# Kernel tuning notes

Measured on AMD Instinct MI355X. Metric: run time of the kernel, lower is better.

Reference implementation:

```python
import jax, jax.numpy as jnp
import numpy as np

T, B, D, H = 512, 64, 1024, 1024


def setup_inputs() -> dict:
    key = jax.random.key(0)
    ks = jax.random.split(key, 7)
    stdv = 1.0 / np.sqrt(H)
    u = lambda k, shape: jax.random.uniform(k, shape, jnp.float32, -stdv, stdv)
    return {
        "x": jax.random.normal(ks[0], (T, B, D), jnp.float32),
        "h0": jax.random.normal(ks[1], (B, H), jnp.float32),
        "c0": jax.random.normal(ks[2], (B, H), jnp.float32),
        "w_ih": u(ks[3], (4 * H, D)),
        "b_ih": u(ks[4], (4 * H,)),
        "w_hh": u(ks[5], (4 * H, H)),
        "b_hh": u(ks[6], (4 * H,)),
    }


def reference(x, h0, c0, w_ih, b_ih, w_hh, b_hh):
    # Precompute input projection for all timesteps in one big GEMM: [T,B,4H]
    gates_x = jnp.einsum("tbd,gd->tbg", x, w_ih) + b_ih

    def step(carry, gx_t):
        h, c = carry
        gates = gx_t + h @ w_hh.T + b_hh  # [B, 4H]
        i_in, f_in, g_in, o_in = jnp.split(gates, 4, axis=1)
        i_t = jax.nn.sigmoid(i_in)
        f_t = jax.nn.sigmoid(f_in)
        g_t = jnp.tanh(g_in)
        o_t = jax.nn.sigmoid(o_in)
        c_t = f_t * c + i_t * g_t
        h_t = o_t * jnp.tanh(c_t)
        return (h_t, c_t), h_t

    (h_n, c_n), hs = jax.lax.scan(step, (h0, c0), gates_x)
    # output: [T, B, H]; final states: [B, H]
    return hs, h_n, c_n
```

## Files before the change

### kernel.cpp

```cpp
#include <hip/hip_runtime.h>

#define TT 512
#define NB 64
#define DD 1024
#define NG 4096

typedef __attribute__((ext_vector_type(8))) __bf16 bf16x8;
typedef __attribute__((ext_vector_type(4))) float f32x4;

#define WC_OFF   0ul
#define HBUF_OFF 16777216ul
#define BIAS_OFF (HBUF_OFF + 262144ul)
#define CNT_OFF  (BIAS_OFF + 16384ul)
#define XBF_OFF  (CNT_OFF + 8192ul)
#define WS_FULL  (XBF_OFF + 67108864ul)

__device__ __forceinline__ unsigned short f2bf(float f) {
  unsigned int u = __float_as_uint(f);
  u += 0x7fffu + ((u >> 16) & 1u);
  return (unsigned short)(u >> 16);
}

__global__ void prep_kernel(const float* __restrict__ x, const float* __restrict__ h0,
                            const float* __restrict__ w_ih, const float* __restrict__ b_ih,
                            const float* __restrict__ w_hh, const float* __restrict__ b_hh,
                            unsigned char* __restrict__ ws, int use_xbf) {
  unsigned short* Wc  = (unsigned short*)(ws + WC_OFF);
  unsigned short* hb  = (unsigned short*)(ws + HBUF_OFF);
  float* bias         = (float*)(ws + BIAS_OFF);
  int* cnt            = (int*)(ws + CNT_OFF);
  unsigned short* xbf = (unsigned short*)(ws + XBF_OFF);
  long tid = (long)blockIdx.x * blockDim.x + threadIdx.x;
  long stride = (long)gridDim.x * blockDim.x;
  for (long i = tid; i < (long)NG * 2048; i += stride) {
    int r = (int)(i >> 11), k = (int)(i & 2047);
    float v = (k < 1024) ? w_ih[(long)r * 1024 + k] : w_hh[(long)r * 1024 + (k - 1024)];
    Wc[i] = f2bf(v);
  }
  for (long i = tid; i < NG; i += stride) bias[i] = b_ih[i] + b_hh[i];
  for (long i = tid; i < NB * DD; i += stride) hb[65536 + i] = f2bf(h0[i]);
  for (long i = tid; i < 4 * TT; i += stride) cnt[i] = 0;
  if (use_xbf) {
    for (long i = tid; i < (long)TT * NB * DD; i += stride) xbf[i] = f2bf(x[i]);
  }
}

__launch_bounds__(512, 2)
__global__ void lstm_kernel(const float* __restrict__ x, const float* __restrict__ c0,
                            float* __restrict__ out, unsigned char* __restrict__ ws,
                            int use_xbf) {
  __shared__ unsigned short A[16 * 2056];
  __shared__ float red[8 * 16 * 64];
  __shared__ float bias_l[64];
  __shared__ float c_l[256];
  __shared__ unsigned short hstage[256];

  const unsigned short* Wc   = (const unsigned short*)(ws + WC_OFF);
  unsigned int* hb32         = (unsigned int*)(ws + HBUF_OFF);
  const float* bias          = (const float*)(ws + BIAS_OFF);
  int* cnt                   = (int*)(ws + CNT_OFF);
  const unsigned short* xbf  = (const unsigned short*)(ws + XBF_OFF);

  const int tid = threadIdx.x;
  const int bg = blockIdx.x >> 6;
  const int cg = blockIdx.x & 63;
  const int m0 = bg << 4;
  const int j0 = cg << 4;
  const int wv = tid >> 6;
  const int lane = tid & 63;
  const int ln = lane & 15;
  const int lq = lane >> 4;

  bf16x8 wreg[32];
  {
    const int k0 = wv * 256 + lq * 8;
#pragma unroll
    for (int c = 0; c < 4; ++c) {
      const unsigned short* wp = Wc + (long)(c * 1024 + j0 + ln) * 2048 + k0;
#pragma unroll
      for (int ks = 0; ks < 8; ++ks)
        wreg[c * 8 + ks] = *reinterpret_cast<const bf16x8*>(wp + ks * 32);
    }
  }
  if (tid < 64) bias_l[tid] = bias[(tid >> 4) * 1024 + j0 + (tid & 15)];
  if (tid < 256) c_l[tid] = c0[(m0 + (tid >> 4)) * DD + j0 + (tid & 15)];

  int* mycnt = cnt + bg * TT;
  unsigned int* const A32 = (unsigned int*)A;

#pragma unroll 1
  for (int t = 0; t < TT; ++t) {
    unsigned int* hwr32       = hb32 + (t & 1) * 32768;
    const unsigned int* hrd32 = hb32 + ((t + 1) & 1) * 32768;

    if (use_xbf) {
      const unsigned short* xs = xbf + ((long)t * NB + m0) * DD;
#pragma unroll
      for (int it = 0; it < 4; ++it) {
        int cid = tid + it * 512;
        int row = cid >> 7, ci = (cid & 127) << 3;
        *(uint4*)(A + row * 2056 + ci) = *(const uint4*)(xs + row * DD + ci);
      }
    } else {
      const float* xs = x + ((long)t * NB + m0) * DD;
#pragma unroll
      for (int it = 0; it < 4; ++it) {
        int cid = tid + it * 512;
        int row = cid >> 7, ci = (cid & 127) << 3;
        const float* p = xs + row * DD + ci;
        float4 f0 = *(const float4*)p;
        float4 f1 = *(const float4*)(p + 4);
        uint4 pk;
        pk.x = (unsigned)f2bf(f0.x) | ((unsigned)f2bf(f0.y) << 16);
        pk.y = (unsigned)f2bf(f0.z) | ((unsigned)f2bf(f0.w) << 16);
        pk.z = (unsigned)f2bf(f1.x) | ((unsigned)f2bf(f1.y) << 16);
        pk.w = (unsigned)f2bf(f1.z) | ((unsigned)f2bf(f1.w) << 16);
        *(uint4*)(A + row * 2056 + ci) = pk;
      }
    }

    if (t > 0) {
      if (tid == 0) {
        while (__hip_atomic_load(mycnt + (t - 1), __ATOMIC_RELAXED,
                                 __HIP_MEMORY_SCOPE_AGENT) < 64)
          __builtin_amdgcn_s_sleep(2);
      }
      __syncthreads();
    }

#pragma unroll 8
    for (int it = 0; it < 16; ++it) {
      int cid = tid + it * 512;
      int row = cid >> 9;
      int wi = cid & 511;
      unsigned int v = __hip_atomic_load(hrd32 + (m0 + row) * 512 + wi,
                                         __ATOMIC_RELAXED, __HIP_MEMORY_SCOPE_AGENT);
      A32[row * 1028 + 512 + wi] = v;
    }
    __syncthreads();

    f32x4 acc0 = {0.f, 0.f, 0.f, 0.f}, acc1 = acc0, acc2 = acc0, acc3 = acc0;
    const unsigned short* ap = A + ln * 2056 + wv * 256 + lq * 8;
#pragma unroll
    for (int ks = 0; ks < 8; ++ks) {
      bf16x8 af = *reinterpret_cast<const bf16x8*>(ap + ks * 32);
      acc0 = __builtin_amdgcn_mfma_f32_16x16x32_bf16(af, wreg[ks],      acc0, 0, 0, 0);
      acc1 = __builtin_amdgcn_mfma_f32_16x16x32_bf16(af, wreg[8 + ks],  acc1, 0, 0, 0);
      acc2 = __builtin_amdgcn_mfma_f32_16x16x32_bf16(af, wreg[16 + ks], acc2, 0, 0, 0);
      acc3 = __builtin_amdgcn_mfma_f32_16x16x32_bf16(af, wreg[24 + ks], acc3, 0, 0, 0);
    }
#pragma unroll
    for (int r = 0; r < 4; ++r) {
      float* rp = red + (wv * 16 + lq * 4 + r) * 64 + ln;
      rp[0] = acc0[r]; rp[16] = acc1[r]; rp[32] = acc2[r]; rp[48] = acc3[r];
    }
    __syncthreads();

    if (tid < 256) {
      const int mm = tid >> 4, jj = tid & 15;
      float s0 = bias_l[jj], s1 = bias_l[16 + jj], s2 = bias_l[32 + jj], s3 = bias_l[48 + jj];
#pragma unroll
      for (int w = 0; w < 8; ++w) {
        const float* rp = red + (w * 16 + mm) * 64 + jj;
        s0 += rp[0]; s1 += rp[16]; s2 += rp[32]; s3 += rp[48];
      }
      float ig = 1.f / (1.f + __expf(-s0));
      float fg = 1.f / (1.f + __expf(-s1));
      float gg = 1.f - 2.f / (__expf(2.f * s2) + 1.f);
      float og = 1.f / (1.f + __expf(-s3));
      float cn = fg * c_l[tid] + ig * gg;
      c_l[tid] = cn;
      float hv = og * (1.f - 2.f / (__expf(2.f * cn) + 1.f));
      const int hoff = (m0 + mm) * DD + j0 + jj;
      out[(long)t * 65536 + hoff] = hv;
      hstage[tid] = f2bf(hv);
      if (t == TT - 1) {
        out[(long)TT * 65536 + hoff] = hv;
        out[(long)TT * 65536 + 65536 + hoff] = cn;
      }
    }
    __syncthreads();

    if (tid < 128) {
      const int row = tid >> 3, wo = tid & 7;
      const unsigned short* hs = hstage + row * 16 + wo * 2;
      unsigned int v = (unsigned int)hs[0] | ((unsigned int)hs[1] << 16);
      __hip_atomic_store(hwr32 + (m0 + row) * 512 + (j0 >> 1) + wo, v,
                         __ATOMIC_RELAXED, __HIP_MEMORY_SCOPE_AGENT);
    }
    __syncthreads();
    if (tid == 0) {
      asm volatile("s_waitcnt vmcnt(0)" ::: "memory");
      __hip_atomic_fetch_add(mycnt + t, 1, __ATOMIC_RELAXED, __HIP_MEMORY_SCOPE_AGENT);
    }
  }
}

extern "C" void kernel_launch(void* const* d_in, const int* in_sizes, int n_in,
                              void* d_out, int out_size, void* d_ws, size_t ws_size,
                              hipStream_t stream) {
  const float* x    = (const float*)d_in[0];
  const float* h0   = (const float*)d_in[1];
  const float* c0   = (const float*)d_in[2];
  const float* w_ih = (const float*)d_in[3];
  const float* b_ih = (const float*)d_in[4];
  const float* w_hh = (const float*)d_in[5];
  const float* b_hh = (const float*)d_in[6];
  float* out = (float*)d_out;
  unsigned char* ws = (unsigned char*)d_ws;
  int use_xbf = (ws_size >= WS_FULL) ? 1 : 0;

  hipLaunchKernelGGL(prep_kernel, dim3(2048), dim3(256), 0, stream,
                     x, h0, w_ih, b_ih, w_hh, b_hh, ws, use_xbf);

  void* args[] = { (void*)&x, (void*)&c0, (void*)&out, (void*)&ws, (void*)&use_xbf };
  hipLaunchCooperativeKernel(reinterpret_cast<void*>(lstm_kernel),
                             dim3(256), dim3(512), args, 0, stream);
}
```

Measured before the change: 3.560 ms.

## Load LSTM operands directly into registers and use per-block flags instead of counters

The LDS staging of x and h is removed. Each wave now loads its MFMA A-fragments straight from global memory into registers, and the next timestep's x is prefetched while the current step computes. The shared step counter with its block-wide barriers is replaced by per-block flag words, which every wave polls with __all. The reduction buffer is double-buffered so one barrier per step is enough, and wave 0 alone runs the vectorized gate math with the cell state held in registers. This is meant to cut barriers and LDS traffic on the serial recurrence path, at the cost of more register pressure and subtler memory-ordering assumptions.

```diff
diff --git a/kernel.cpp b/kernel.cpp
--- a/kernel.cpp
+++ b/kernel.cpp
@@ -45,20 +45,19 @@
   }
 }
 
+#define MFMA16 __builtin_amdgcn_mfma_f32_16x16x32_bf16
+
 __launch_bounds__(512, 2)
 __global__ void lstm_kernel(const float* __restrict__ x, const float* __restrict__ c0,
                             float* __restrict__ out, unsigned char* __restrict__ ws,
                             int use_xbf) {
-  __shared__ unsigned short A[16 * 2056];
-  __shared__ float red[8 * 16 * 64];
+  __shared__ __align__(16) float red[2][8][16][68];
   __shared__ float bias_l[64];
-  __shared__ float c_l[256];
-  __shared__ unsigned short hstage[256];
 
   const unsigned short* Wc   = (const unsigned short*)(ws + WC_OFF);
-  unsigned int* hb32         = (unsigned int*)(ws + HBUF_OFF);
+  unsigned long long* hb64   = (unsigned long long*)(ws + HBUF_OFF);
   const float* bias          = (const float*)(ws + BIAS_OFF);
-  int* cnt                   = (int*)(ws + CNT_OFF);
+  int* flags                 = (int*)(ws + CNT_OFF);
   const unsigned short* xbf  = (const unsigned short*)(ws + XBF_OFF);
 
   const int tid = threadIdx.x;
@@ -71,127 +70,155 @@
   const int ln = lane & 15;
   const int lq = lane >> 4;
 
-  bf16x8 wreg[32];
+  bf16x8 wx[16], wh[16];
   {
-    const int k0 = wv * 256 + lq * 8;
-#pragma unroll
-    for (int c = 0; c < 4; ++c) {
-      const unsigned short* wp = Wc + (long)(c * 1024 + j0 + ln) * 2048 + k0;
-#pragma unroll
-      for (int ks = 0; ks < 8; ++ks)
-        wreg[c * 8 + ks] = *reinterpret_cast<const bf16x8*>(wp + ks * 32);
+    const int kx = wv * 128 + lq * 8;
+#pragma unroll
+    for (int g = 0; g < 4; ++g) {
+      const unsigned short* wp = Wc + (long)(g * 1024 + j0 + ln) * 2048 + kx;
+#pragma unroll
+      for (int ks = 0; ks < 4; ++ks) {
+        wx[g * 4 + ks] = *reinterpret_cast<const bf16x8*>(wp + ks * 32);
+        wh[g * 4 + ks] = *reinterpret_cast<const bf16x8*>(wp + 1024 + ks * 32);
+      }
     }
   }
   if (tid < 64) bias_l[tid] = bias[(tid >> 4) * 1024 + j0 + (tid & 15)];
-  if (tid < 256) c_l[tid] = c0[(m0 + (tid >> 4)) * DD + j0 + (tid & 15)];
-
-  int* mycnt = cnt + bg * TT;
-  unsigned int* const A32 = (unsigned int*)A;
-
-#pragma unroll 1
-  for (int t = 0; t < TT; ++t) {
-    unsigned int* hwr32       = hb32 + (t & 1) * 32768;
-    const unsigned int* hrd32 = hb32 + ((t + 1) & 1) * 32768;
-
+
+  const int mm = lane >> 2;
+  const int jj0 = (lane & 3) << 2;
+  float cr0 = 0.f, cr1 = 0.f, cr2 = 0.f, cr3 = 0.f;
+  if (wv == 0) {
+    const float4 cv = *(const float4*)(c0 + (long)(m0 + mm) * DD + j0 + jj0);
+    cr0 = cv.x; cr1 = cv.y; cr2 = cv.z; cr3 = cv.w;
+  }
+
+  const long xbase = (long)(m0 + ln) * DD + wv * 128 + lq * 8;
+  uint4 xcur[4];
+  auto load_x = [&](int tt) {
     if (use_xbf) {
-      const unsigned short* xs = xbf + ((long)t * NB + m0) * DD;
-#pragma unroll
-      for (int it = 0; it < 4; ++it) {
-        int cid = tid + it * 512;
-        int row = cid >> 7, ci = (cid & 127) << 3;
-        *(uint4*)(A + row * 2056 + ci) = *(const uint4*)(xs + row * DD + ci);
-      }
+      const unsigned short* xp = xbf + (long)tt * (NB * DD) + xbase;
+#pragma unroll
+      for (int ks = 0; ks < 4; ++ks)
+        xcur[ks] = *reinterpret_cast<const uint4*>(xp + ks * 32);
     } else {
-      const float* xs = x + ((long)t * NB + m0) * DD;
-#pragma unroll
-      for (int it = 0; it < 4; ++it) {
-        int cid = tid + it * 512;
-        int row = cid >> 7, ci = (cid & 127) << 3;
-        const float* p = xs + row * DD + ci;
-        float4 f0 = *(const float4*)p;
-        float4 f1 = *(const float4*)(p + 4);
+      const float* xp = x + (long)tt * (NB * DD) + xbase;
+#pragma unroll
+      for (int ks = 0; ks < 4; ++ks) {
+        float4 f0 = *reinterpret_cast<const float4*>(xp + ks * 32);
+        float4 f1 = *reinterpret_cast<const float4*>(xp + ks * 32 + 4);
         uint4 pk;
         pk.x = (unsigned)f2bf(f0.x) | ((unsigned)f2bf(f0.y) << 16);
         pk.y = (unsigned)f2bf(f0.z) | ((unsigned)f2bf(f0.w) << 16);
         pk.z = (unsigned)f2bf(f1.x) | ((unsigned)f2bf(f1.y) << 16);
         pk.w = (unsigned)f2bf(f1.z) | ((unsigned)f2bf(f1.w) << 16);
-        *(uint4*)(A + row * 2056 + ci) = pk;
-      }
-    }
+        xcur[ks] = pk;
+      }
+    }
+  };
+  load_x(0);
+
+  const int fl0 = (bg * 64 + wv * 8 + (lane & 7)) * 8;
+  const int myflag = (bg * 64 + cg) * 8;
+  const int hrow = (m0 + ln) * 256 + wv * 32 + lq * 2;
+
+#pragma unroll 1
+  for (int t = 0; t < TT; ++t) {
+    const int rb = t & 1;
 
     if (t > 0) {
-      if (tid == 0) {
-        while (__hip_atomic_load(mycnt + (t - 1), __ATOMIC_RELAXED,
-                                 __HIP_MEMORY_SCOPE_AGENT) < 64)
-          __builtin_amdgcn_s_sleep(2);
-      }
-      __syncthreads();
-    }
-
-#pragma unroll 8
-    for (int it = 0; it < 16; ++it) {
-      int cid = tid + it * 512;
-      int row = cid >> 9;
-      int wi = cid & 511;
-      unsigned int v = __hip_atomic_load(hrd32 + (m0 + row) * 512 + wi,
-                                         __ATOMIC_RELAXED, __HIP_MEMORY_SCOPE_AGENT);
-      A32[row * 1028 + 512 + wi] = v;
-    }
-    __syncthreads();
-
-    f32x4 acc0 = {0.f, 0.f, 0.f, 0.f}, acc1 = acc0, acc2 = acc0, acc3 = acc0;
-    const unsigned short* ap = A + ln * 2056 + wv * 256 + lq * 8;
-#pragma unroll
-    for (int ks = 0; ks < 8; ++ks) {
-      bf16x8 af = *reinterpret_cast<const bf16x8*>(ap + ks * 32);
-      acc0 = __builtin_amdgcn_mfma_f32_16x16x32_bf16(af, wreg[ks],      acc0, 0, 0, 0);
-      acc1 = __builtin_amdgcn_mfma_f32_16x16x32_bf16(af, wreg[8 + ks],  acc1, 0, 0, 0);
-      acc2 = __builtin_amdgcn_mfma_f32_16x16x32_bf16(af, wreg[16 + ks], acc2, 0, 0, 0);
-      acc3 = __builtin_amdgcn_mfma_f32_16x16x32_bf16(af, wreg[24 + ks], acc3, 0, 0, 0);
-    }
+      while (true) {
+        int v = __hip_atomic_load(flags + fl0, __ATOMIC_RELAXED, __HIP_MEMORY_SCOPE_AGENT);
+        if (__all(v >= t)) break;
+        __builtin_amdgcn_s_sleep(1);
+      }
+    }
+    asm volatile("" ::: "memory");
+
+    const unsigned long long* hp = hb64 + ((t + 1) & 1) * 16384 + hrow;
+    unsigned long long hq[8];
+#pragma unroll
+    for (int ks = 0; ks < 4; ++ks) {
+      hq[2 * ks]     = __hip_atomic_load(hp + ks * 8,     __ATOMIC_RELAXED, __HIP_MEMORY_SCOPE_AGENT);
+      hq[2 * ks + 1] = __hip_atomic_load(hp + ks * 8 + 1, __ATOMIC_RELAXED, __HIP_MEMORY_SCOPE_AGENT);
+    }
+
+    f32x4 a0 = {0.f, 0.f, 0.f, 0.f}, a1 = a0, a2 = a0, a3 = a0;
+#pragma unroll
+    for (int ks = 0; ks < 4; ++ks) {
+      bf16x8 af = __builtin_bit_cast(bf16x8, xcur[ks]);
+      a0 = MFMA16(af, wx[ks],      a0, 0, 0, 0);
+      a1 = MFMA16(af, wx[4 + ks],  a1, 0, 0, 0);
+      a2 = MFMA16(af, wx[8 + ks],  a2, 0, 0, 0);
+      a3 = MFMA16(af, wx[12 + ks], a3, 0, 0, 0);
+    }
+    if (wv != 0 && t + 1 < TT) load_x(t + 1);
+
+#pragma unroll
+    for (int ks = 0; ks < 4; ++ks) {
+      union { unsigned long long q[2]; bf16x8 v; } uu;
+      uu.q[0] = hq[2 * ks]; uu.q[1] = hq[2 * ks + 1];
+      a0 = MFMA16(uu.v, wh[ks],      a0, 0, 0, 0);
+      a1 = MFMA16(uu.v, wh[4 + ks],  a1, 0, 0, 0);
+      a2 = MFMA16(uu.v, wh[8 + ks],  a2, 0, 0, 0);
+      a3 = MFMA16(uu.v, wh[12 + ks], a3, 0, 0, 0);
+    }
+
 #pragma unroll
     for (int r = 0; r < 4; ++r) {
-      float* rp = red + (wv * 16 + lq * 4 + r) * 64 + ln;
-      rp[0] = acc0[r]; rp[16] = acc1[r]; rp[32] = acc2[r]; rp[48] = acc3[r];
-    }
-    __syncthreads();
-
-    if (tid < 256) {
-      const int mm = tid >> 4, jj = tid & 15;
-      float s0 = bias_l[jj], s1 = bias_l[16 + jj], s2 = bias_l[32 + jj], s3 = bias_l[48 + jj];
+      float* rp = &red[rb][wv][lq * 4 + r][ln];
+      rp[0] = a0[r]; rp[16] = a1[r]; rp[32] = a2[r]; rp[48] = a3[r];
+    }
+
+    asm volatile("s_waitcnt lgkmcnt(0)" ::: "memory");
+    __builtin_amdgcn_s_barrier();
+    __builtin_amdgcn_sched_barrier(0);
+
+    if (wv == 0) {
+      __builtin_amdgcn_s_setprio(1);
+      f32x4 s0 = *(const f32x4*)&bias_l[jj0];
+      f32x4 s1 = *(const f32x4*)&bias_l[16 + jj0];
+      f32x4 s2 = *(const f32x4*)&bias_l[32 + jj0];
+      f32x4 s3 = *(const f32x4*)&bias_l[48 + jj0];
 #pragma unroll
       for (int w = 0; w < 8; ++w) {
-        const float* rp = red + (w * 16 + mm) * 64 + jj;
-        s0 += rp[0]; s1 += rp[16]; s2 += rp[32]; s3 += rp[48];
-      }
-      float ig = 1.f / (1.f + __expf(-s0));
-      float fg = 1.f / (1.f + __expf(-s1));
-      float gg = 1.f - 2.f / (__expf(2.f * s2) + 1.f);
-      float og = 1.f / (1.f + __expf(-s3));
-      float cn = fg * c_l[tid] + ig * gg;
-      c_l[tid] = cn;
-      float hv = og * (1.f - 2.f / (__expf(2.f * cn) + 1.f));
-      const int hoff = (m0 + mm) * DD + j0 + jj;
-      out[(long)t * 65536 + hoff] = hv;
-      hstage[tid] = f2bf(hv);
+        const float* rp = &red[rb][w][mm][jj0];
+        s0 += *(const f32x4*)(rp);
+        s1 += *(const f32x4*)(rp + 16);
+        s2 += *(const f32x4*)(rp + 32);
+        s3 += *(const f32x4*)(rp + 48);
+      }
+      float cold[4] = {cr0, cr1, cr2, cr3};
+      float hv[4], cn[4];
+#pragma unroll
+      for (int e = 0; e < 4; ++e) {
+        float ig = 1.f / (1.f + __expf(-s0[e]));
+        float fg = 1.f / (1.f + __expf(-s1[e]));
+        float gg = 1.f - 2.f / (__expf(2.f * s2[e]) + 1.f);
+        float og = 1.f / (1.f + __expf(-s3[e]));
+        float c2 = fg * cold[e] + ig * gg;
+        cn[e] = c2;
+        hv[e] = og * (1.f - 2.f / (__expf(2.f * c2) + 1.f));
+      }
+      cr0 = cn[0]; cr1 = cn[1]; cr2 = cn[2]; cr3 = cn[3];
+
+      const long ho = (long)(m0 + mm) * 1024 + j0 + jj0;
+      *(float4*)(out + (long)t * 65536 + ho) = make_float4(hv[0], hv[1], hv[2], hv[3]);
       if (t == TT - 1) {
-        out[(long)TT * 65536 + hoff] = hv;
-        out[(long)TT * 65536 + 65536 + hoff] = cn;
-      }
-    }
-    __syncthreads();
-
-    if (tid < 128) {
-      const int row = tid >> 3, wo = tid & 7;
-      const unsigned short* hs = hstage + row * 16 + wo * 2;
-      unsigned int v = (unsigned int)hs[0] | ((unsigned int)hs[1] << 16);
-      __hip_atomic_store(hwr32 + (m0 + row) * 512 + (j0 >> 1) + wo, v,
+        *(float4*)(out + (long)TT * 65536 + ho) = make_float4(hv[0], hv[1], hv[2], hv[3]);
+        *(float4*)(out + (long)TT * 65536 + 65536 + ho) = make_float4(cn[0], cn[1], cn[2], cn[3]);
+      }
+      unsigned long long hqo = (unsigned long long)f2bf(hv[0])
+        | ((unsigned long long)f2bf(hv[1]) << 16)
+        | ((unsigned long long)f2bf(hv[2]) << 32)
+        | ((unsigned long long)f2bf(hv[3]) << 48);
+      __hip_atomic_store(hb64 + rb * 16384 + (m0 + mm) * 256 + ((j0 + jj0) >> 2), hqo,
                          __ATOMIC_RELAXED, __HIP_MEMORY_SCOPE_AGENT);
-    }
-    __syncthreads();
-    if (tid == 0) {
       asm volatile("s_waitcnt vmcnt(0)" ::: "memory");
-      __hip_atomic_fetch_add(mycnt + t, 1, __ATOMIC_RELAXED, __HIP_MEMORY_SCOPE_AGENT);
+      if (lane == 0)
+        __hip_atomic_store(flags + myflag, t + 1, __ATOMIC_RELAXED, __HIP_MEMORY_SCOPE_AGENT);
+      __builtin_amdgcn_s_setprio(0);
+      if (t + 1 < TT) load_x(t + 1);
     }
   }
 }
```

Result: faster. 3.190 ms (-10.4%).
